# Kernel optimization log

Measured on AMD Instinct MI355X. Metric: run time of the kernel, lower is better.

The kernel has to match this reference:

```python
import jax, jax.numpy as jnp
import numpy as np

N_HEAD = 16


def setup_inputs() -> dict:
    key = jax.random.key(0)
    ks = jax.random.split(key, 5)
    B, T, C = 4, 2048, 1024
    s = 0.02
    return {
        "x": jax.random.normal(ks[0], (B, T, C), dtype=jnp.float32),
        "Wq": jax.random.normal(ks[1], (C, C), dtype=jnp.float32) * s,
        "Wk": jax.random.normal(ks[2], (C, C), dtype=jnp.float32) * s,
        "Wv": jax.random.normal(ks[3], (C, C), dtype=jnp.float32) * s,
        "Wp": jax.random.normal(ks[4], (C, C), dtype=jnp.float32) * s,
    }


def reference(x, Wq, Wk, Wv, Wp):
    B, T, C = x.shape
    H = N_HEAD
    D = C // H
    # torch Linear(bias=False): x @ W.T
    q = (x @ Wq.T).reshape(B, T, H, D).transpose(0, 2, 1, 3)  # [B,H,T,D]
    k = (x @ Wk.T).reshape(B, T, H, D).transpose(0, 2, 1, 3)
    v = (x @ Wv.T).reshape(B, T, H, D).transpose(0, 2, 1, 3)
    scale = 1.0 / jnp.sqrt(jnp.float32(D))
    att = jnp.einsum("bhqd,bhkd->bhqk", q, k) * scale  # [B,H,T,T]
    causal = jnp.tril(jnp.ones((T, T), dtype=bool))
    att = jnp.where(causal, att, jnp.float32(-jnp.inf))
    att = jax.nn.softmax(att, axis=-1)
    y = jnp.einsum("bhqk,bhkd->bhqd", att, v)  # [B,H,T,D]
    y = y.transpose(0, 2, 1, 3).reshape(B, T, C)
    return y @ Wp.T
```

## Files before the change

kernel.cpp:

```cpp
#include <hip/hip_runtime.h>
#include <hip/hip_bf16.h>
#include <math.h>

typedef __hip_bfloat16 bf16;
typedef __attribute__((ext_vector_type(8))) short short8;
typedef __attribute__((ext_vector_type(4))) float f32x4;
typedef __attribute__((ext_vector_type(2))) unsigned uint2v;
typedef __attribute__((ext_vector_type(4))) unsigned uint4v;

#define MFMA_BF16(a, b, c) __builtin_amdgcn_mfma_f32_16x16x32_bf16((a), (b), (c), 0, 0, 0)

__device__ __forceinline__ void async_copy16(const bf16* g, bf16* l) {
  __builtin_amdgcn_global_load_lds(
      (const __attribute__((address_space(1))) void*)g,
      (__attribute__((address_space(3))) void*)l,
      16, 0, 0);
}

__device__ __forceinline__ unsigned short f2bf_bits(float f) {
  bf16 h = __float2bfloat16(f);
  return *reinterpret_cast<unsigned short*>(&h);
}

__device__ __forceinline__ unsigned cvt_pk_bf16(float lo, float hi) {
  unsigned r;
  asm("v_cvt_pk_bf16_f32 %0, %1, %2" : "=v"(r) : "v"(lo), "v"(hi));
  return r;
}

__global__ __launch_bounds__(256) void cvt_all(const float* __restrict__ x,
                                               const float* __restrict__ wq,
                                               const float* __restrict__ wk,
                                               const float* __restrict__ wv,
                                               const float* __restrict__ wp,
                                               bf16* __restrict__ xb, bf16* __restrict__ wqb,
                                               bf16* __restrict__ wkb, bf16* __restrict__ wvb,
                                               bf16* __restrict__ wpb) {
  const int bid = blockIdx.x;
  const float* in;
  bf16* out;
  int off;
  float scale = 1.0f;
  if (bid < 8192) {
    in = x; out = xb; off = bid;
  } else if (bid < 9216) {
    in = wq; out = wqb; off = bid - 8192;
    scale = 0.180336880111112f;
  } else if (bid < 10240) {
    in = wk; out = wkb; off = bid - 9216;
  } else if (bid < 11264) {
    in = wv; out = wvb; off = bid - 10240;
  } else {
    in = wp; out = wpb; off = bid - 11264;
  }
  const int i = off * 256 + threadIdx.x;
  float4 v = reinterpret_cast<const float4*>(in)[i];
  ushort4 u;
  u.x = f2bf_bits(v.x * scale);
  u.y = f2bf_bits(v.y * scale);
  u.z = f2bf_bits(v.z * scale);
  u.w = f2bf_bits(v.w * scale);
  reinterpret_cast<ushort4*>(out)[i] = u;
}

__device__ __forceinline__ void gemm_core(const bf16* __restrict__ A,
                                          const bf16* __restrict__ W,
                                          bf16* As, bf16* Bs, f32x4 (&acc)[4][4]) {
  const int tid = threadIdx.x;
  const int lane = tid & 63;
  const int l15 = lane & 15;
  const int quad = lane >> 4;
  const int wave = tid >> 6;
  const int wm = (wave >> 1) * 64;
  const int wn = (wave & 1) * 64;
  const int K = 1024;

  const f32x4 zero = {0.f, 0.f, 0.f, 0.f};
#pragma unroll
  for (int i = 0; i < 4; ++i)
#pragma unroll
    for (int j = 0; j < 4; ++j) acc[i][j] = zero;

  const int srow = tid >> 2;
  const int scol = (tid & 3) * 8;
  const bf16* ga = A + (size_t)(blockIdx.y * 128 + srow) * K + scol;
  const bf16* gb = W + (size_t)(blockIdx.x * 128 + srow) * K + scol;
  bf16* lA = As + tid * 8;
  bf16* lB = Bs + tid * 8;

  for (int kt = 0; kt < 32; ++kt) {
    const int k0 = kt * 32;
    async_copy16(ga + k0, lA);
    async_copy16(ga + k0 + 64 * K, lA + 2048);
    async_copy16(gb + k0, lB);
    async_copy16(gb + k0 + 64 * K, lB + 2048);
    __syncthreads();
    short8 afr[4], bfr[4];
#pragma unroll
    for (int i = 0; i < 4; ++i)
      afr[i] = *reinterpret_cast<const short8*>(As + (wm + i * 16 + l15) * 32 + quad * 8);
#pragma unroll
    for (int j = 0; j < 4; ++j)
      bfr[j] = *reinterpret_cast<const short8*>(Bs + (wn + j * 16 + l15) * 32 + quad * 8);
#pragma unroll
    for (int i = 0; i < 4; ++i)
#pragma unroll
      for (int j = 0; j < 4; ++j) acc[i][j] = MFMA_BF16(afr[i], bfr[j], acc[i][j]);
    __syncthreads();
  }
}

__global__ __launch_bounds__(256) void gemm_qkv(const bf16* __restrict__ x,
                                                const bf16* __restrict__ wq,
                                                const bf16* __restrict__ wk,
                                                const bf16* __restrict__ wv,
                                                bf16* __restrict__ q, bf16* __restrict__ k,
                                                bf16* __restrict__ vt) {
  __shared__ __align__(16) bf16 As[128 * 32];
  __shared__ __align__(16) bf16 Bs[128 * 32];
  const bf16* W = (blockIdx.z == 0) ? wq : (blockIdx.z == 1) ? wk : wv;
  f32x4 acc[4][4];
  gemm_core(x, W, As, Bs, acc);
  const int tid = threadIdx.x, lane = tid & 63, l15 = lane & 15, quad = lane >> 4,
            wave = tid >> 6;
  const int wm = (wave >> 1) * 64, wn = (wave & 1) * 64;
  const int rb = blockIdx.y * 128 + wm + quad * 4;
  const int cb = blockIdx.x * 128 + wn + l15;
  if (blockIdx.z == 2) {
#pragma unroll
    for (int i = 0; i < 4; ++i)
#pragma unroll
      for (int j = 0; j < 4; ++j) {
        const int tg = rb + i * 16;
        const int col = cb + j * 16;
        const int b = tg >> 11, tl = tg & 2047;
        const int tls = (tl & ~12) | ((tl & 4) << 1) | ((tl & 8) >> 1);
        ushort4 pk;
        pk.x = f2bf_bits(acc[i][j][0]);
        pk.y = f2bf_bits(acc[i][j][1]);
        pk.z = f2bf_bits(acc[i][j][2]);
        pk.w = f2bf_bits(acc[i][j][3]);
        *reinterpret_cast<ushort4*>(&vt[((size_t)(b * 1024 + col)) * 2048 + tls]) = pk;
      }
  } else {
    bf16* C = (blockIdx.z == 0) ? q : k;
#pragma unroll
    for (int i = 0; i < 4; ++i)
#pragma unroll
      for (int j = 0; j < 4; ++j)
#pragma unroll
        for (int r = 0; r < 4; ++r)
          C[(size_t)(rb + i * 16 + r) * 1024 + cb + j * 16] = __float2bfloat16(acc[i][j][r]);
  }
}

__global__ __launch_bounds__(256) void gemm_proj(const bf16* __restrict__ y,
                                                 const bf16* __restrict__ wp,
                                                 float* __restrict__ outp) {
  __shared__ __align__(16) bf16 As[128 * 32];
  __shared__ __align__(16) bf16 Bs[128 * 32];
  f32x4 acc[4][4];
  gemm_core(y, wp, As, Bs, acc);
  const int tid = threadIdx.x, lane = tid & 63, l15 = lane & 15, quad = lane >> 4,
            wave = tid >> 6;
  const int wm = (wave >> 1) * 64, wn = (wave & 1) * 64;
  const int rb = blockIdx.y * 128 + wm + quad * 4;
  const int cb = blockIdx.x * 128 + wn + l15;
#pragma unroll
  for (int i = 0; i < 4; ++i)
#pragma unroll
    for (int j = 0; j < 4; ++j)
#pragma unroll
      for (int r = 0; r < 4; ++r)
        outp[(size_t)(rb + i * 16 + r) * 1024 + cb + j * 16] = acc[i][j][r];
}

__global__ __launch_bounds__(256) void attn(const bf16* __restrict__ qb,
                                            const bf16* __restrict__ kb,
                                            const bf16* __restrict__ vt,
                                            bf16* __restrict__ yb) {
  __shared__ __align__(16) bf16 Ks[2][2048];
  __shared__ __align__(16) bf16 Vs[2][2048];
  const int tid = threadIdx.x;
  const int lane = tid & 63, l15 = lane & 15, quad = lane >> 4, wave = tid >> 6;
  const int p = blockIdx.y;
  const int bh = blockIdx.x;
  const int b = bh >> 4, h = bh & 15;
  const size_t rowbase = (size_t)b * 2048;
  const int cb = h * 64;

  const int tlo = p, thi = 31 - p;
  const int gq0[2] = {tlo * 64 + wave * 16, thi * 64 + wave * 16};

  short8 aq[2][2];
#pragma unroll
  for (int g = 0; g < 2; ++g) {
    const bf16* qp = qb + (rowbase + gq0[g] + l15) * 1024 + cb + quad * 8;
    aq[g][0] = *reinterpret_cast<const short8*>(qp);
    aq[g][1] = *reinterpret_cast<const short8*>(qp + 32);
  }

  short8 ones;
#pragma unroll
  for (int i = 0; i < 8; ++i) ones[i] = (short)0x3F80;

  f32x4 o[2][4], l4[2];
  const f32x4 zero = {0.f, 0.f, 0.f, 0.f};
#pragma unroll
  for (int g = 0; g < 2; ++g) {
#pragma unroll
    for (int dt = 0; dt < 4; ++dt) o[g][dt] = zero;
    l4[g] = zero;
  }

  const int sdq = (((tid & 3) ^ ((tid >> 2) & 3) ^ ((tid >> 4) & 3))) * 8;
  const bf16* kg = kb + (rowbase + ((tid & 127) >> 2)) * 1024 + cb + (tid >> 7) * 32 + sdq;
  const bf16* vg = vt + ((size_t)bh * 64 + (tid >> 2)) * 2048 + sdq;
  const int csw = (quad ^ (l15 & 3) ^ ((l15 >> 2) & 3)) * 8;

  const int nkt = 2 * thi + 2;
  async_copy16(kg, &Ks[0][tid * 8]);
  async_copy16(vg, &Vs[0][tid * 8]);

  for (int kt = 0; kt < nkt; ++kt) {
    const int buf = kt & 1;
    __syncthreads();
    if (kt + 1 < nkt) {
      async_copy16(kg + (size_t)(kt + 1) * 32 * 1024, &Ks[buf ^ 1][tid * 8]);
      async_copy16(vg + (kt + 1) * 32, &Vs[buf ^ 1][tid * 8]);
    }
    const int k0g = kt * 32;
    if (k0g > gq0[1] + 15) continue;

    short8 bk[2][2];
#pragma unroll
    for (int j = 0; j < 2; ++j)
#pragma unroll
      for (int ks = 0; ks < 2; ++ks)
        bk[j][ks] = *reinterpret_cast<const short8*>(
            &Ks[buf][ks * 1024 + (j * 16 + l15) * 32 + csw]);
    short8 av[4];
#pragma unroll
    for (int dt = 0; dt < 4; ++dt)
      av[dt] = *reinterpret_cast<const short8*>(&Vs[buf][(dt * 16 + l15) * 32 + csw]);

#pragma unroll
    for (int g = 0; g < 2; ++g) {
      if (k0g > gq0[g] + 15) continue;
      f32x4 st[2];
#pragma unroll
      for (int j = 0; j < 2; ++j) {
        st[j] = MFMA_BF16(bk[j][0], aq[g][0], zero);
        st[j] = MFMA_BF16(bk[j][1], aq[g][1], st[j]);
      }
      const bool need_mask = (k0g + 31 > gq0[g]);
      unsigned w[2][2];
#pragma unroll
      for (int j = 0; j < 2; ++j) {
        float pw[4];
#pragma unroll
        for (int r = 0; r < 4; ++r) {
          float val = st[j][r];
          if (need_mask && (k0g + j * 16 + quad * 4 + r) > (gq0[g] + l15))
            val = -INFINITY;
          pw[r] = __builtin_amdgcn_exp2f(val);
        }
        w[j][0] = cvt_pk_bf16(pw[0], pw[1]);
        w[j][1] = cvt_pk_bf16(pw[2], pw[3]);
      }
      uint2v s0 = __builtin_amdgcn_permlane32_swap(w[0][0], w[1][0], false, false);
      uint2v s1 = __builtin_amdgcn_permlane32_swap(w[0][1], w[1][1], false, false);
      uint4v u;
      u[0] = s0[0];
      u[1] = s1[0];
      u[2] = s0[1];
      u[3] = s1[1];
      const short8 bp = __builtin_bit_cast(short8, u);
#pragma unroll
      for (int dt = 0; dt < 4; ++dt) o[g][dt] = MFMA_BF16(av[dt], bp, o[g][dt]);
      l4[g] = MFMA_BF16(ones, bp, l4[g]);
    }
  }

#pragma unroll
  for (int g = 0; g < 2; ++g) {
    const float invl = 1.f / l4[g][0];
    bf16* yp = yb + (rowbase + gq0[g] + l15) * 1024 + cb + quad * 4;
#pragma unroll
    for (int dt = 0; dt < 4; ++dt) {
      ushort4 pk;
      pk.x = f2bf_bits(o[g][dt][0] * invl);
      pk.y = f2bf_bits(o[g][dt][1] * invl);
      pk.z = f2bf_bits(o[g][dt][2] * invl);
      pk.w = f2bf_bits(o[g][dt][3] * invl);
      *reinterpret_cast<ushort4*>(&yp[dt * 16]) = pk;
    }
  }
}

extern "C" void kernel_launch(void* const* d_in, const int* in_sizes, int n_in,
                              void* d_out, int out_size, void* d_ws, size_t ws_size,
                              hipStream_t stream) {
  const float* x = (const float*)d_in[0];
  const float* Wq = (const float*)d_in[1];
  const float* Wk = (const float*)d_in[2];
  const float* Wv = (const float*)d_in[3];
  const float* Wp = (const float*)d_in[4];
  float* out = (float*)d_out;

  const size_t MB = 1024 * 1024;
  char* ws = (char*)d_ws;
  bf16* xb = (bf16*)(ws);
  bf16* qb = (bf16*)(ws + 16 * MB);
  bf16* kb = (bf16*)(ws + 32 * MB);
  bf16* vtb = (bf16*)(ws + 48 * MB);
  bf16* wqb = (bf16*)(ws + 64 * MB);
  bf16* wkb = (bf16*)(ws + 66 * MB);
  bf16* wvb = (bf16*)(ws + 68 * MB);
  bf16* wpb = (bf16*)(ws + 70 * MB);
  bf16* yb = xb;

  cvt_all<<<12288, 256, 0, stream>>>(x, Wq, Wk, Wv, Wp, xb, wqb, wkb, wvb, wpb);
  gemm_qkv<<<dim3(8, 64, 3), 256, 0, stream>>>(xb, wqb, wkb, wvb, qb, kb, vtb);
  attn<<<dim3(64, 16), 256, 0, stream>>>(qb, kb, vtb, yb);
  gemm_proj<<<dim3(8, 64), 256, 0, stream>>>(yb, wpb, out);
}
```

Measured before the change: 280.5 us.

## Pipeline GEMMs with 4-stage async LDS buffering, 256x128 tiles, swizzled LDS

```diff
diff --git a/kernel.cpp b/kernel.cpp
--- a/kernel.cpp
+++ b/kernel.cpp
@@ -63,116 +63,139 @@
   reinterpret_cast<ushort4*>(out)[i] = u;
 }
 
-__device__ __forceinline__ void gemm_core(const bf16* __restrict__ A,
-                                          const bf16* __restrict__ W,
-                                          bf16* As, bf16* Bs, f32x4 (&acc)[4][4]) {
-  const int tid = threadIdx.x;
-  const int lane = tid & 63;
+__device__ __forceinline__ void gemm_core256(const bf16* __restrict__ A,
+                                             const bf16* __restrict__ W,
+                                             f32x4 (&acc)[4][4]) {
+  __shared__ __align__(16) bf16 L[4][12288];
+  const int t = threadIdx.x;
+  const int lane = t & 63;
   const int l15 = lane & 15;
-  const int quad = lane >> 4;
-  const int wave = tid >> 6;
+  const int quad = (lane >> 4) & 3;
+  const int wave = t >> 6;
   const int wm = (wave >> 1) * 64;
   const int wn = (wave & 1) * 64;
   const int K = 1024;
 
   const f32x4 zero = {0.f, 0.f, 0.f, 0.f};
 #pragma unroll
-  for (int i = 0; i < 4; ++i)
-#pragma unroll
-    for (int j = 0; j < 4; ++j) acc[i][j] = zero;
-
-  const int srow = tid >> 2;
-  const int scol = (tid & 3) * 8;
-  const bf16* ga = A + (size_t)(blockIdx.y * 128 + srow) * K + scol;
-  const bf16* gb = W + (size_t)(blockIdx.x * 128 + srow) * K + scol;
-  bf16* lA = As + tid * 8;
-  bf16* lB = Bs + tid * 8;
-
-  for (int kt = 0; kt < 32; ++kt) {
-    const int k0 = kt * 32;
-    async_copy16(ga + k0, lA);
-    async_copy16(ga + k0 + 64 * K, lA + 2048);
-    async_copy16(gb + k0, lB);
-    async_copy16(gb + k0 + 64 * K, lB + 2048);
-    __syncthreads();
-    short8 afr[4], bfr[4];
-#pragma unroll
-    for (int i = 0; i < 4; ++i)
-      afr[i] = *reinterpret_cast<const short8*>(As + (wm + i * 16 + l15) * 32 + quad * 8);
-#pragma unroll
-    for (int j = 0; j < 4; ++j)
-      bfr[j] = *reinterpret_cast<const short8*>(Bs + (wn + j * 16 + l15) * 32 + quad * 8);
-#pragma unroll
-    for (int i = 0; i < 4; ++i)
-#pragma unroll
-      for (int j = 0; j < 4; ++j) acc[i][j] = MFMA_BF16(afr[i], bfr[j], acc[i][j]);
-    __syncthreads();
-  }
-}
-
-__global__ __launch_bounds__(256) void gemm_qkv(const bf16* __restrict__ x,
-                                                const bf16* __restrict__ wq,
-                                                const bf16* __restrict__ wk,
-                                                const bf16* __restrict__ wv,
-                                                bf16* __restrict__ q, bf16* __restrict__ k,
-                                                bf16* __restrict__ vt) {
-  __shared__ __align__(16) bf16 As[128 * 32];
-  __shared__ __align__(16) bf16 Bs[128 * 32];
+  for (int m = 0; m < 4; ++m)
+#pragma unroll
+    for (int n = 0; n < 4; ++n) acc[m][n] = zero;
+
+  const int srow = t >> 2;
+  const int schunk = ((t & 3) ^ ((t >> 3) & 3)) * 8;
+  const bf16* ga0 = A + (size_t)(blockIdx.y * 256 + srow) * K + schunk;
+  const bf16* ga1 = ga0 + (size_t)128 * K;
+  const bf16* gb0 = W + (size_t)(blockIdx.x * 128 + srow) * K + schunk;
+
+  const int fsw = (quad ^ ((l15 >> 1) & 3)) * 8;
+  const int arow = (wm + l15) * 32 + fsw;
+  const int brow = 8192 + (wn + l15) * 32 + fsw;
+
+#pragma unroll
+  for (int kt = 0; kt < 3; ++kt) {
+    bf16* Ld = &L[kt][0];
+    async_copy16(ga0 + kt * 32, Ld + t * 8);
+    async_copy16(ga1 + kt * 32, Ld + 4096 + t * 8);
+    async_copy16(gb0 + kt * 32, Ld + 8192 + t * 8);
+  }
+  asm volatile("s_waitcnt vmcnt(6)" ::: "memory");
+  __builtin_amdgcn_s_barrier();
+
+  for (int T = 0; T < 32; ++T) {
+    const bf16* Lb = &L[T & 3][0];
+    short8 af[4], bfr[4];
+#pragma unroll
+    for (int m = 0; m < 4; ++m)
+      af[m] = *reinterpret_cast<const short8*>(Lb + arow + m * 512);
+#pragma unroll
+    for (int n = 0; n < 4; ++n)
+      bfr[n] = *reinterpret_cast<const short8*>(Lb + brow + n * 512);
+    if (T <= 28) {
+      bf16* Ld = &L[(T + 3) & 3][0];
+      async_copy16(ga0 + (T + 3) * 32, Ld + t * 8);
+      async_copy16(ga1 + (T + 3) * 32, Ld + 4096 + t * 8);
+      async_copy16(gb0 + (T + 3) * 32, Ld + 8192 + t * 8);
+    }
+    if (T < 29)
+      asm volatile("s_waitcnt vmcnt(6)" ::: "memory");
+    else if (T == 29)
+      asm volatile("s_waitcnt vmcnt(3)" ::: "memory");
+    else
+      asm volatile("s_waitcnt vmcnt(0)" ::: "memory");
+    __builtin_amdgcn_s_barrier();
+    asm volatile("s_waitcnt lgkmcnt(0)" ::: "memory");
+    __builtin_amdgcn_sched_barrier(0);
+    __builtin_amdgcn_s_setprio(1);
+#pragma unroll
+    for (int m = 0; m < 4; ++m)
+#pragma unroll
+      for (int n = 0; n < 4; ++n) acc[m][n] = MFMA_BF16(af[m], bfr[n], acc[m][n]);
+    __builtin_amdgcn_s_setprio(0);
+    __builtin_amdgcn_sched_barrier(0);
+    __builtin_amdgcn_s_barrier();
+  }
+}
+
+__global__ __launch_bounds__(512, 2) void gemm_qkv(const bf16* __restrict__ x,
+                                                   const bf16* __restrict__ wq,
+                                                   const bf16* __restrict__ wk,
+                                                   const bf16* __restrict__ wv,
+                                                   bf16* __restrict__ q, bf16* __restrict__ k,
+                                                   bf16* __restrict__ vt) {
   const bf16* W = (blockIdx.z == 0) ? wq : (blockIdx.z == 1) ? wk : wv;
   f32x4 acc[4][4];
-  gemm_core(x, W, As, Bs, acc);
-  const int tid = threadIdx.x, lane = tid & 63, l15 = lane & 15, quad = lane >> 4,
-            wave = tid >> 6;
+  gemm_core256(x, W, acc);
+  const int t = threadIdx.x, lane = t & 63, l15 = lane & 15, quad = (lane >> 4) & 3,
+            wave = t >> 6;
   const int wm = (wave >> 1) * 64, wn = (wave & 1) * 64;
-  const int rb = blockIdx.y * 128 + wm + quad * 4;
-  const int cb = blockIdx.x * 128 + wn + l15;
+  const int rb = blockIdx.y * 256 + wm + quad * 4;
+  const int cbb = blockIdx.x * 128 + wn + l15;
   if (blockIdx.z == 2) {
 #pragma unroll
-    for (int i = 0; i < 4; ++i)
-#pragma unroll
-      for (int j = 0; j < 4; ++j) {
-        const int tg = rb + i * 16;
-        const int col = cb + j * 16;
+    for (int m = 0; m < 4; ++m)
+#pragma unroll
+      for (int n = 0; n < 4; ++n) {
+        const int tg = rb + m * 16;
+        const int col = cbb + n * 16;
         const int b = tg >> 11, tl = tg & 2047;
         const int tls = (tl & ~12) | ((tl & 4) << 1) | ((tl & 8) >> 1);
         ushort4 pk;
-        pk.x = f2bf_bits(acc[i][j][0]);
-        pk.y = f2bf_bits(acc[i][j][1]);
-        pk.z = f2bf_bits(acc[i][j][2]);
-        pk.w = f2bf_bits(acc[i][j][3]);
+        pk.x = f2bf_bits(acc[m][n][0]);
+        pk.y = f2bf_bits(acc[m][n][1]);
+        pk.z = f2bf_bits(acc[m][n][2]);
+        pk.w = f2bf_bits(acc[m][n][3]);
         *reinterpret_cast<ushort4*>(&vt[((size_t)(b * 1024 + col)) * 2048 + tls]) = pk;
       }
   } else {
     bf16* C = (blockIdx.z == 0) ? q : k;
 #pragma unroll
-    for (int i = 0; i < 4; ++i)
-#pragma unroll
-      for (int j = 0; j < 4; ++j)
+    for (int m = 0; m < 4; ++m)
+#pragma unroll
+      for (int n = 0; n < 4; ++n)
 #pragma unroll
         for (int r = 0; r < 4; ++r)
-          C[(size_t)(rb + i * 16 + r) * 1024 + cb + j * 16] = __float2bfloat16(acc[i][j][r]);
-  }
-}
-
-__global__ __launch_bounds__(256) void gemm_proj(const bf16* __restrict__ y,
-                                                 const bf16* __restrict__ wp,
-                                                 float* __restrict__ outp) {
-  __shared__ __align__(16) bf16 As[128 * 32];
-  __shared__ __align__(16) bf16 Bs[128 * 32];
+          C[(size_t)(rb + m * 16 + r) * 1024 + cbb + n * 16] = __float2bfloat16(acc[m][n][r]);
+  }
+}
+
+__global__ __launch_bounds__(512, 2) void gemm_proj(const bf16* __restrict__ y,
+                                                    const bf16* __restrict__ wp,
+                                                    float* __restrict__ outp) {
   f32x4 acc[4][4];
-  gemm_core(y, wp, As, Bs, acc);
-  const int tid = threadIdx.x, lane = tid & 63, l15 = lane & 15, quad = lane >> 4,
-            wave = tid >> 6;
+  gemm_core256(y, wp, acc);
+  const int t = threadIdx.x, lane = t & 63, l15 = lane & 15, quad = (lane >> 4) & 3,
+            wave = t >> 6;
   const int wm = (wave >> 1) * 64, wn = (wave & 1) * 64;
-  const int rb = blockIdx.y * 128 + wm + quad * 4;
-  const int cb = blockIdx.x * 128 + wn + l15;
-#pragma unroll
-  for (int i = 0; i < 4; ++i)
-#pragma unroll
-    for (int j = 0; j < 4; ++j)
+  const int rb = blockIdx.y * 256 + wm + quad * 4;
+  const int cbb = blockIdx.x * 128 + wn + l15;
+#pragma unroll
+  for (int m = 0; m < 4; ++m)
+#pragma unroll
+    for (int n = 0; n < 4; ++n)
 #pragma unroll
       for (int r = 0; r < 4; ++r)
-        outp[(size_t)(rb + i * 16 + r) * 1024 + cb + j * 16] = acc[i][j][r];
+        outp[(size_t)(rb + m * 16 + r) * 1024 + cbb + n * 16] = acc[m][n][r];
 }
 
 __global__ __launch_bounds__(256) void attn(const bf16* __restrict__ qb,
@@ -321,7 +344,7 @@
   bf16* yb = xb;
 
   cvt_all<<<12288, 256, 0, stream>>>(x, Wq, Wk, Wv, Wp, xb, wqb, wkb, wvb, wpb);
-  gemm_qkv<<<dim3(8, 64, 3), 256, 0, stream>>>(xb, wqb, wkb, wvb, qb, kb, vtb);
+  gemm_qkv<<<dim3(8, 32, 3), 512, 0, stream>>>(xb, wqb, wkb, wvb, qb, kb, vtb);
   attn<<<dim3(64, 16), 256, 0, stream>>>(qb, kb, vtb, yb);
-  gemm_proj<<<dim3(8, 64), 256, 0, stream>>>(yb, wpb, out);
-}
+  gemm_proj<<<dim3(8, 32), 512, 0, stream>>>(yb, wpb, out);
+}
```

New measurement: 277.8 us. About the same (-1.0%).
